# Kernel tuning notes

Hardware: AMD Instinct MI355X
Metric: run time of the kernel (lower is better)

Reference implementation:

```python
import jax, jax.numpy as jnp
import numpy as np

N_FEATURES = 32
HIDDEN_DIM = 64
B, T = 512, 1024


def lstm(x, w_ih, w_hh, b_ih, b_hh):
    """PyTorch-compatible single-layer LSTM, batch_first.
    x: [B, T, F_in]; w_ih: [4H, F_in]; w_hh: [4H, H]; b_ih, b_hh: [4H].
    Gate order (PyTorch): i, f, g, o. Returns outputs [B, T, H].
    """
    Bq, Tq, _ = x.shape
    H = w_hh.shape[1]
    # Precompute input contribution for all timesteps (big GEMM, time-parallel)
    x_gates = jnp.einsum('btf,gf->btg', x, w_ih) + b_ih + b_hh  # [B, T, 4H]
    x_gates = jnp.swapaxes(x_gates, 0, 1)  # [T, B, 4H]

    def step(carry, xg):
        h, c = carry
        gates = xg + h @ w_hh.T  # [B, 4H]
        i = jax.nn.sigmoid(gates[:, 0 * H:1 * H])
        f = jax.nn.sigmoid(gates[:, 1 * H:2 * H])
        g = jnp.tanh(gates[:, 2 * H:3 * H])
        o = jax.nn.sigmoid(gates[:, 3 * H:4 * H])
        c = f * c + i * g
        h = o * jnp.tanh(c)
        return (h, c), h

    h0 = jnp.zeros((Bq, H), dtype=x.dtype)
    c0 = jnp.zeros((Bq, H), dtype=x.dtype)
    _, hs = jax.lax.scan(step, (h0, c0), x_gates)  # hs: [T, B, H]
    return jnp.swapaxes(hs, 0, 1)  # [B, T, H]


def setup_inputs() -> dict:
    key = jax.random.key(0)
    ks = jax.random.split(key, 9)
    F, H = N_FEATURES, HIDDEN_DIM
    s_enc = 1.0 / np.sqrt(H)
    s_dec = 1.0 / np.sqrt(F)
    return {
        'x': jax.random.normal(ks[0], (B, T, F), dtype=jnp.float32),
        # encoder: input F -> hidden H
        'enc_w_ih': jax.random.uniform(ks[1], (4 * H, F), jnp.float32, -s_enc, s_enc),
        'enc_w_hh': jax.random.uniform(ks[2], (4 * H, H), jnp.float32, -s_enc, s_enc),
        'enc_b_ih': jax.random.uniform(ks[3], (4 * H,), jnp.float32, -s_enc, s_enc),
        'enc_b_hh': jax.random.uniform(ks[4], (4 * H,), jnp.float32, -s_enc, s_enc),
        # decoder: input H -> hidden F
        'dec_w_ih': jax.random.uniform(ks[5], (4 * F, H), jnp.float32, -s_dec, s_dec),
        'dec_w_hh': jax.random.uniform(ks[6], (4 * F, F), jnp.float32, -s_dec, s_dec),
        'dec_b_ih': jax.random.uniform(ks[7], (4 * F,), jnp.float32, -s_dec, s_dec),
        'dec_b_hh': jax.random.uniform(ks[8], (4 * F,), jnp.float32, -s_dec, s_dec),
    }


def reference(x, enc_w_ih, enc_w_hh, enc_b_ih, enc_b_hh,
              dec_w_ih, dec_w_hh, dec_b_ih, dec_b_hh):
    encoded = lstm(x, enc_w_ih, enc_w_hh, enc_b_ih, enc_b_hh)      # [B, T, H]
    decoded = lstm(encoded, dec_w_ih, dec_w_hh, dec_b_ih, dec_b_hh)  # [B, T, F]
    return decoded
```

## Files before the change

kernel.cpp:

```cpp
#include <hip/hip_runtime.h>
#include <stdint.h>
#include <math.h>

#define TT 1024
#define FF 32
#define HH 64

typedef unsigned int u32;
typedef _Float16 f16;
typedef __attribute__((ext_vector_type(8))) _Float16 half8;
typedef __attribute__((ext_vector_type(4))) float v4f;

__device__ __forceinline__ float fsig(float x) {
    return __builtin_amdgcn_rcpf(1.f + __builtin_amdgcn_exp2f(-1.44269504088896341f * x));
}
__device__ __forceinline__ float ftanh(float x) {
    return 2.f * __builtin_amdgcn_rcpf(1.f + __builtin_amdgcn_exp2f(-2.88539008177792681f * x)) - 1.f;
}

__device__ __forceinline__ half8 ld8h(const float* p) {
    float4 a = *(const float4*)p, b = *(const float4*)(p + 4);
    half8 r;
    r[0] = (f16)a.x; r[1] = (f16)a.y; r[2] = (f16)a.z; r[3] = (f16)a.w;
    r[4] = (f16)b.x; r[5] = (f16)b.y; r[6] = (f16)b.z; r[7] = (f16)b.w;
    return r;
}


__global__ __launch_bounds__(256, 2)
void lstm_ae_mfma(const float* __restrict__ x,
                  const float* __restrict__ ewih, const float* __restrict__ ewhh,
                  const float* __restrict__ ebih, const float* __restrict__ ebhh,
                  const float* __restrict__ dwih, const float* __restrict__ dwhh,
                  const float* __restrict__ dbih, const float* __restrict__ dbhh,
                  float* __restrict__ out)
{
    const int b = blockIdx.x;
    const int t = threadIdx.x;
    const int w = t >> 6;
    const int l = t & 63;
    const int q = l >> 4;
    const int n = l & 15;

    __shared__ __align__(16) f16 Bst[2][2][160];
    __shared__ __align__(16) float xst[2][2048];

    half8 af[6][3];
#pragma unroll
    for (int i = 0; i < 6; ++i) {
        int tile = w * 6 + i;
        if (tile < 16) {
            int r = (n & 3) * 64 + tile * 4 + (n >> 2);
            af[i][0] = ld8h(ewhh + r * 64 + q * 8);
            af[i][1] = ld8h(ewhh + r * 64 + 32 + q * 8);
            af[i][2] = ld8h(ewih + r * 32 + q * 8);
        } else {
            int r = (n & 3) * 32 + (tile - 16) * 4 + (n >> 2);
            af[i][0] = ld8h(dwih + r * 64 + q * 8);
            af[i][1] = ld8h(dwih + r * 64 + 32 + q * 8);
            af[i][2] = ld8h(dwhh + r * 32 + q * 8);
        }
    }

    const int sel = n >> 1;
    const bool act = (n < 12);
    const int tile_s = w * 6 + (sel < 6 ? sel : 0);
    const bool is_enc = (tile_s < 16);
    const int u = is_enc ? (tile_s * 4 + q) : ((tile_s - 16) * 4 + q);

    float b0 = 0.f, b1 = 0.f, b2 = 0.f, b3 = 0.f, c_st = 0.f;
    if (act) {
        if (is_enc) {
            b0 = ebih[u]       + ebhh[u];
            b1 = ebih[64 + u]  + ebhh[64 + u];
            b2 = ebih[128 + u] + ebhh[128 + u];
            b3 = ebih[192 + u] + ebhh[192 + u];
        } else {
            b0 = dbih[u]      + dbhh[u];
            b1 = dbih[32 + u] + dbhh[32 + u];
            b2 = dbih[64 + u] + dbhh[64 + u];
            b3 = dbih[96 + u] + dbhh[96 + u];
        }
    }

    { u32* bz = (u32*)&Bst[0][0][0]; for (int i2 = t; i2 < 2 * 2 * 160 / 2; i2 += 256) bz[i2] = 0u; }
    const float* xb = x + (size_t)b * TT * FF;
    *(float4*)&xst[0][t * 8]     = *(const float4*)(xb + t * 8);
    *(float4*)&xst[0][t * 8 + 4] = *(const float4*)(xb + t * 8 + 4);
    __syncthreads();
    if (t >= 96 && t < 128) Bst[0][0][64 + (t - 96)] = (f16)xst[0][t - 96];
    __syncthreads();

    for (int tt = 0; tt <= TT; ++tt) {
        const int p = tt & 1;

        float4 px0, px1;
        const int cn = (tt >> 6) + 1;
        const bool pf = ((tt & 63) == 0) && (cn < 16);
        if (pf) {
            px0 = *(const float4*)(xb + cn * 2048 + t * 8);
            px1 = *(const float4*)(xb + cn * 2048 + t * 8 + 4);
        }

        const f16* Bp = &Bst[p][0][0];
        const int cb = (n & 1) * 160 + q * 8;
        half8 bf0 = *(const half8*)(Bp + cb);
        half8 bf1 = *(const half8*)(Bp + cb + 32);
        half8 bf2 = *(const half8*)(Bp + cb + 64);
        half8 bf3 = *(const half8*)(Bp + cb + 96);

        v4f zero = {0.f, 0.f, 0.f, 0.f};
        v4f acc[6];
#pragma unroll
        for (int i = 0; i < 6; ++i)
            acc[i] = __builtin_amdgcn_mfma_f32_16x16x32_f16(af[i][2], (w * 6 + i < 16) ? bf2 : bf3,
                                                            zero, 0, 0, 0);
#pragma unroll
        for (int i = 0; i < 6; ++i)
            acc[i] = __builtin_amdgcn_mfma_f32_16x16x32_f16(af[i][0], bf0, acc[i], 0, 0, 0);
#pragma unroll
        for (int i = 0; i < 6; ++i)
            acc[i] = __builtin_amdgcn_mfma_f32_16x16x32_f16(af[i][1], bf1, acc[i], 0, 0, 0);

        v4f u_ = acc[0];
#pragma unroll
        for (int i = 1; i < 6; ++i) if (sel == i) u_ = acc[i];

        v4f s_;
#pragma unroll
        for (int e = 0; e < 4; ++e) {
            int tmp = __builtin_amdgcn_update_dpp(0, __float_as_int(u_[e]), 0xB1, 0xF, 0xF, true);
            s_[e] = u_[e] + __int_as_float(tmp);
        }

        f16* Bw = &Bst[p ^ 1][0][0];
        if (act && (is_enc ? (tt < TT) : (tt >= 1))) {
            float i_ = fsig(s_[0] + b0);
            float f_ = fsig(s_[1] + b1);
            float g_ = ftanh(s_[2] + b2);
            float o_ = fsig(s_[3] + b3);
            c_st = f_ * c_st + i_ * g_;
            float h = o_ * ftanh(c_st);
            f16 hi = (f16)h;
            f16 lo = (f16)(h - (float)hi);
            const int kk = is_enc ? u : (96 + u);
            Bw[(n & 1) * 160 + kk] = (n & 1) ? lo : hi;
            if (!is_enc && !(n & 1))
                out[(size_t)b * TT * FF + (size_t)(tt - 1) * FF + u] = h;
        } else if (n == 12 || n == 13) {
            int st = tt + 1;
            if (st < TT) {
                int j = w * 8 + q * 2 + (n - 12);
                Bw[64 + j] = (f16)xst[(st >> 6) & 1][(st & 63) * 32 + j];
            }
        }

        if (pf) {
            *(float4*)&xst[cn & 1][t * 8]     = px0;
            *(float4*)&xst[cn & 1][t * 8 + 4] = px1;
        }

        asm volatile("s_waitcnt lgkmcnt(0)" ::: "memory");
        __builtin_amdgcn_s_barrier();
        __builtin_amdgcn_sched_barrier(0);
    }
}

extern "C" void kernel_launch(void* const* d_in, const int* in_sizes, int n_in,
                              void* d_out, int out_size, void* d_ws, size_t ws_size,
                              hipStream_t stream) {
    (void)in_sizes; (void)n_in; (void)out_size; (void)d_ws; (void)ws_size;
    lstm_ae_mfma<<<512, 256, 0, stream>>>((const float*)d_in[0],
                                          (const float*)d_in[1], (const float*)d_in[2],
                                          (const float*)d_in[3], (const float*)d_in[4],
                                          (const float*)d_in[5], (const float*)d_in[6],
                                          (const float*)d_in[7], (const float*)d_in[8],
                                          (float*)d_out);
}
```

Before: 741.4 us.

## Process two sequences per block with 8 waves, three gate tiles per wave

Each block now handles two batch sequences with 512 threads (8 waves) instead of one sequence with 4 waves. Each wave holds 3 weight tiles instead of 6, and the MFMA B operand packs both sequences' hi/lo columns so a single MFMA serves both sequences. The goal is to shorten the per-timestep serial chain, since there are fewer MFMAs per wave, while keeping total work the same on 256 blocks. The cost is a larger block barrier across 8 waves at every step and fewer blocks available to fill the CUs.

```diff
diff --git a/kernel.cpp b/kernel.cpp
--- a/kernel.cpp
+++ b/kernel.cpp
@@ -5,6 +5,7 @@
 #define TT 1024
 #define FF 32
 #define HH 64
+#define CSTR 176
 
 typedef unsigned int u32;
 typedef _Float16 f16;
@@ -26,8 +27,13 @@
     return r;
 }
 
+__device__ __forceinline__ float pairsum(float v) {
+    int t = __builtin_amdgcn_update_dpp(0, __float_as_int(v), 0xB1, 0xF, 0xF, true);
+    return v + __int_as_float(t);
+}
 
-__global__ __launch_bounds__(256, 2)
+
+__global__ __launch_bounds__(512, 2)
 void lstm_ae_mfma(const float* __restrict__ x,
                   const float* __restrict__ ewih, const float* __restrict__ ewhh,
                   const float* __restrict__ ebih, const float* __restrict__ ebhh,
@@ -35,20 +41,20 @@
                   const float* __restrict__ dbih, const float* __restrict__ dbhh,
                   float* __restrict__ out)
 {
-    const int b = blockIdx.x;
+    const int b2 = blockIdx.x;
     const int t = threadIdx.x;
     const int w = t >> 6;
     const int l = t & 63;
     const int q = l >> 4;
     const int n = l & 15;
 
-    __shared__ __align__(16) f16 Bst[2][2][160];
-    __shared__ __align__(16) float xst[2][2048];
+    __shared__ __align__(16) f16 Bst[2][4][CSTR];
+    __shared__ __align__(16) float xst[2][2][2048];
 
-    half8 af[6][3];
+    half8 af[3][3];
 #pragma unroll
-    for (int i = 0; i < 6; ++i) {
-        int tile = w * 6 + i;
+    for (int i = 0; i < 3; ++i) {
+        int tile = w * 3 + i;
         if (tile < 16) {
             int r = (n & 3) * 64 + tile * 4 + (n >> 2);
             af[i][0] = ld8h(ewhh + r * 64 + q * 8);
@@ -62,34 +68,46 @@
         }
     }
 
-    const int sel = n >> 1;
-    const bool act = (n < 12);
-    const int tile_s = w * 6 + (sel < 6 ? sel : 0);
-    const bool is_enc = (tile_s < 16);
-    const int u = is_enc ? (tile_s * 4 + q) : ((tile_s - 16) * 4 + q);
+    const int pr   = n >> 1;
+    const int sq   = pr & 1;
+    const int slot = pr >> 1;
+    const bool act = (slot < 3);
+    const int T1   = w * 3 + (act ? slot : 0);
+    const bool e1  = (T1 < 16);
+    const int u1i  = e1 ? T1 * 4 + q : (T1 - 16) * 4 + q;
+    const int wk1  = (sq * 2 + (n & 1)) * CSTR + (e1 ? u1i : 96 + u1i);
 
-    float b0 = 0.f, b1 = 0.f, b2 = 0.f, b3 = 0.f, c_st = 0.f;
+    float b0 = 0.f, b1 = 0.f, b2b = 0.f, b3 = 0.f, c1 = 0.f;
     if (act) {
-        if (is_enc) {
-            b0 = ebih[u]       + ebhh[u];
-            b1 = ebih[64 + u]  + ebhh[64 + u];
-            b2 = ebih[128 + u] + ebhh[128 + u];
-            b3 = ebih[192 + u] + ebhh[192 + u];
+        if (e1) {
+            b0  = ebih[u1i]       + ebhh[u1i];
+            b1  = ebih[64 + u1i]  + ebhh[64 + u1i];
+            b2b = ebih[128 + u1i] + ebhh[128 + u1i];
+            b3  = ebih[192 + u1i] + ebhh[192 + u1i];
         } else {
-            b0 = dbih[u]      + dbhh[u];
-            b1 = dbih[32 + u] + dbhh[32 + u];
-            b2 = dbih[64 + u] + dbhh[64 + u];
-            b3 = dbih[96 + u] + dbhh[96 + u];
+            b0  = dbih[u1i]      + dbhh[u1i];
+            b1  = dbih[32 + u1i] + dbhh[32 + u1i];
+            b2b = dbih[64 + u1i] + dbhh[64 + u1i];
+            b3  = dbih[96 + u1i] + dbhh[96 + u1i];
         }
     }
 
-    { u32* bz = (u32*)&Bst[0][0][0]; for (int i2 = t; i2 < 2 * 2 * 160 / 2; i2 += 256) bz[i2] = 0u; }
-    const float* xb = x + (size_t)b * TT * FF;
-    *(float4*)&xst[0][t * 8]     = *(const float4*)(xb + t * 8);
-    *(float4*)&xst[0][t * 8 + 4] = *(const float4*)(xb + t * 8 + 4);
+    { u32* bz = (u32*)&Bst[0][0][0]; for (int i2 = t; i2 < 2 * 4 * CSTR / 2; i2 += 512) bz[i2] = 0u; }
+    const float* xb0 = x + (size_t)(2 * b2) * TT * FF;
+    const float* xb1 = xb0 + TT * FF;
+    {
+        const int ts = t >> 8;
+        const int ti = t & 255;
+        const float* xbm = ts ? xb1 : xb0;
+        *(float4*)&xst[ts][0][ti * 8]     = *(const float4*)(xbm + ti * 8);
+        *(float4*)&xst[ts][0][ti * 8 + 4] = *(const float4*)(xbm + ti * 8 + 4);
+    }
     __syncthreads();
-    if (t >= 96 && t < 128) Bst[0][0][64 + (t - 96)] = (f16)xst[0][t - 96];
+    if (t < 32)       Bst[0][0][64 + t]        = (f16)xst[0][0][t];
+    else if (t < 64)  Bst[0][2][64 + (t - 32)] = (f16)xst[1][0][t - 32];
     __syncthreads();
+
+    float* outp = out + (size_t)(2 * b2 + sq) * TT * FF;
 
     for (int tt = 0; tt <= TT; ++tt) {
         const int p = tt & 1;
@@ -98,66 +116,66 @@
         const int cn = (tt >> 6) + 1;
         const bool pf = ((tt & 63) == 0) && (cn < 16);
         if (pf) {
-            px0 = *(const float4*)(xb + cn * 2048 + t * 8);
-            px1 = *(const float4*)(xb + cn * 2048 + t * 8 + 4);
+            const float* xbm = (t >> 8) ? xb1 : xb0;
+            px0 = *(const float4*)(xbm + cn * 2048 + (t & 255) * 8);
+            px1 = *(const float4*)(xbm + cn * 2048 + (t & 255) * 8 + 4);
         }
 
         const f16* Bp = &Bst[p][0][0];
-        const int cb = (n & 1) * 160 + q * 8;
+        const int cb = (n & 3) * CSTR + q * 8;
         half8 bf0 = *(const half8*)(Bp + cb);
         half8 bf1 = *(const half8*)(Bp + cb + 32);
         half8 bf2 = *(const half8*)(Bp + cb + 64);
         half8 bf3 = *(const half8*)(Bp + cb + 96);
 
         v4f zero = {0.f, 0.f, 0.f, 0.f};
-        v4f acc[6];
+        v4f acc[3];
 #pragma unroll
-        for (int i = 0; i < 6; ++i)
-            acc[i] = __builtin_amdgcn_mfma_f32_16x16x32_f16(af[i][2], (w * 6 + i < 16) ? bf2 : bf3,
+        for (int i = 0; i < 3; ++i)
+            acc[i] = __builtin_amdgcn_mfma_f32_16x16x32_f16(af[i][2], (w * 3 + i < 16) ? bf2 : bf3,
                                                             zero, 0, 0, 0);
 #pragma unroll
-        for (int i = 0; i < 6; ++i)
+        for (int i = 0; i < 3; ++i)
             acc[i] = __builtin_amdgcn_mfma_f32_16x16x32_f16(af[i][0], bf0, acc[i], 0, 0, 0);
 #pragma unroll
-        for (int i = 0; i < 6; ++i)
+        for (int i = 0; i < 3; ++i)
             acc[i] = __builtin_amdgcn_mfma_f32_16x16x32_f16(af[i][1], bf1, acc[i], 0, 0, 0);
 
         v4f u_ = acc[0];
-#pragma unroll
-        for (int i = 1; i < 6; ++i) if (sel == i) u_ = acc[i];
+        if (slot == 1) u_ = acc[1];
+        if (slot == 2) u_ = acc[2];
 
         v4f s_;
 #pragma unroll
-        for (int e = 0; e < 4; ++e) {
-            int tmp = __builtin_amdgcn_update_dpp(0, __float_as_int(u_[e]), 0xB1, 0xF, 0xF, true);
-            s_[e] = u_[e] + __int_as_float(tmp);
-        }
+        for (int e = 0; e < 4; ++e) s_[e] = pairsum(u_[e]);
 
         f16* Bw = &Bst[p ^ 1][0][0];
-        if (act && (is_enc ? (tt < TT) : (tt >= 1))) {
+
+        if (act && (e1 ? (tt < TT) : (tt >= 1))) {
             float i_ = fsig(s_[0] + b0);
             float f_ = fsig(s_[1] + b1);
-            float g_ = ftanh(s_[2] + b2);
+            float g_ = ftanh(s_[2] + b2b);
             float o_ = fsig(s_[3] + b3);
-            c_st = f_ * c_st + i_ * g_;
-            float h = o_ * ftanh(c_st);
+            c1 = f_ * c1 + i_ * g_;
+            float h = o_ * ftanh(c1);
             f16 hi = (f16)h;
             f16 lo = (f16)(h - (float)hi);
-            const int kk = is_enc ? u : (96 + u);
-            Bw[(n & 1) * 160 + kk] = (n & 1) ? lo : hi;
-            if (!is_enc && !(n & 1))
-                out[(size_t)b * TT * FF + (size_t)(tt - 1) * FF + u] = h;
-        } else if (n == 12 || n == 13) {
+            Bw[wk1] = (n & 1) ? lo : hi;
+            if (!e1 && !(n & 1))
+                outp[(size_t)(tt - 1) * FF + u1i] = h;
+        }
+        if (n == 12 || n == 14) {
             int st = tt + 1;
             if (st < TT) {
-                int j = w * 8 + q * 2 + (n - 12);
-                Bw[64 + j] = (f16)xst[(st >> 6) & 1][(st & 63) * 32 + j];
+                int sx = (n - 12) >> 1;
+                int jj = w * 4 + q;
+                Bw[(sx * 2) * CSTR + 64 + jj] = (f16)xst[sx][(st >> 6) & 1][(st & 63) * 32 + jj];
             }
         }
 
         if (pf) {
-            *(float4*)&xst[cn & 1][t * 8]     = px0;
-            *(float4*)&xst[cn & 1][t * 8 + 4] = px1;
+            *(float4*)&xst[t >> 8][cn & 1][(t & 255) * 8]     = px0;
+            *(float4*)&xst[t >> 8][cn & 1][(t & 255) * 8 + 4] = px1;
         }
 
         asm volatile("s_waitcnt lgkmcnt(0)" ::: "memory");
@@ -170,7 +188,7 @@
                               void* d_out, int out_size, void* d_ws, size_t ws_size,
                               hipStream_t stream) {
     (void)in_sizes; (void)n_in; (void)out_size; (void)d_ws; (void)ws_size;
-    lstm_ae_mfma<<<512, 256, 0, stream>>>((const float*)d_in[0],
+    lstm_ae_mfma<<<256, 512, 0, stream>>>((const float*)d_in[0],
                                           (const float*)d_in[1], (const float*)d_in[2],
                                           (const float*)d_in[3], (const float*)d_in[4],
                                           (const float*)d_in[5], (const float*)d_in[6],
```

Result: slower. 1.520 ms (+105.1%).
